# Optimization experiments

Hardware: AMD Instinct MI355X
Metric: run time of the kernel (lower is better)

## Reference

```python
import jax, jax.numpy as jnp
import numpy as np

B, N, D, IN_NF, OUT_NF, H, L = 64, 64, 3, 8, 1, 128, 4
BN = B * N
E = B * N * N


def setup_inputs() -> dict:
    key = jax.random.key(0)
    ks = jax.random.split(key, 12)
    g = lambda k, shape, s=0.05: jax.random.normal(k, shape, jnp.float32) * s
    z = lambda *shape: jnp.zeros(shape, jnp.float32)
    return {
        "xh": jax.random.normal(ks[0], (B, N, D + IN_NF), jnp.float32),
        "node_mask": jnp.ones((B, N, 1), jnp.float32),
        "edge_mask": jnp.ones((B, N * N, 1), jnp.float32),
        "emb_w": g(ks[1], (IN_NF, H)), "emb_b": z(H),
        "out_w": g(ks[2], (H, OUT_NF)), "out_b": z(OUT_NF),
        "ew1": g(ks[3], (L, 2 * H + 2, H)), "eb1": z(L, H),
        "ew2": g(ks[4], (L, H, H)), "eb2": z(L, H),
        "nw1": g(ks[5], (L, 2 * H, H)), "nb1": z(L, H),
        "nw2": g(ks[6], (L, H, H)), "nb2": z(L, H),
        "cw1": g(ks[7], (L, H, H)), "cb1": z(L, H),
        "cw2": g(ks[8], (L, H, 1), 0.001),  # xavier gain 0.001, no bias
    }


def _edges():
    # fully-connected edges within each graph block (matches get_adj_matrix)
    ii = jnp.repeat(jnp.arange(N, dtype=jnp.int32), N)  # source i
    jj = jnp.tile(jnp.arange(N, dtype=jnp.int32), N)    # target j
    offs = (jnp.arange(B, dtype=jnp.int32) * N)[:, None]
    row = (offs + ii[None, :]).reshape(-1)  # [E]
    col = (offs + jj[None, :]).reshape(-1)  # [E]
    return row, col


def reference(xh, node_mask, edge_mask, emb_w, emb_b, out_w, out_b,
              ew1, eb1, ew2, eb2, nw1, nb1, nw2, nb2, cw1, cb1, cw2):
    silu = jax.nn.silu
    row, col = _edges()
    nm = node_mask.reshape(BN, 1)
    em = edge_mask.reshape(E, 1)

    x = xh[:, :, :D].reshape(BN, D) * nm           # coordinates
    h = xh[:, :, D:].reshape(BN, IN_NF) * nm       # node features
    # static per-graph edge attribute: squared distance at input coords
    edge_attr = jnp.sum((x[row] - x[col]) ** 2, axis=1, keepdims=True)  # [E,1]

    h = h @ emb_w + emb_b  # embedding

    for l in range(L):
        coord_diff = x[row] - x[col]                            # [E,D]
        radial = jnp.sum(coord_diff ** 2, axis=1, keepdims=True)  # [E,1]
        coord_diff = coord_diff / (jnp.sqrt(radial + 1e-8) + 1.0)  # norm_diff

        # edge MLP: cat(h_i, h_j, radial, edge_attr) -> SiLU stack
        e_in = jnp.concatenate([h[row], h[col], radial, edge_attr], axis=1)
        m = silu(silu(e_in @ ew1[l] + eb1[l]) @ ew2[l] + eb2[l])  # [E,H]
        m = m * em

        # coordinate update (tanh=False): coord_diff * coord_mlp(m)
        trans = coord_diff * (silu(m @ cw1[l] + cb1[l]) @ cw2[l])  # [E,D]
        trans = trans * em
        x = x + jax.ops.segment_sum(trans, row, num_segments=BN)

        # node update with residual (recurrent=True)
        agg = jax.ops.segment_sum(m, row, num_segments=BN)       # [BN,H]
        n_in = jnp.concatenate([h, agg], axis=1)
        h = h + (silu(n_in @ nw1[l] + nb1[l]) @ nw2[l] + nb2[l])
        h = h * nm

    h = (h @ out_w + out_b) * nm                    # embedding_out + node mask
    return h.reshape(B, N, OUT_NF).mean(axis=1)     # [B, out_nf]
```

## Files before the change

kernel.cpp:

```cpp
#include <hip/hip_runtime.h>
#include <math.h>


#define NB 64
#define NN 64
#define DD 3
#define INNF 8
#define HH 128
#define LL 4
#define BNODES (NB * NN)

typedef __attribute__((ext_vector_type(8))) short bf16x8;
typedef __attribute__((ext_vector_type(4))) float f32x4;

__device__ __forceinline__ float silu_f(float v) {
    float e = __expf(-v);
    return v * __builtin_amdgcn_rcpf(1.0f + e);
}

__device__ __forceinline__ short f2bf(float v) {
    unsigned u = __builtin_bit_cast(unsigned, v);
    u += 0x7fffu + ((u >> 16) & 1u);
    return (short)(u >> 16);
}

__global__ void prep_kernel(const float* __restrict__ xh, const float* __restrict__ nm,
                            const float* __restrict__ emb_w, const float* __restrict__ emb_b,
                            float* __restrict__ x, float* __restrict__ x0, float* __restrict__ h) {
    const int v = blockIdx.x;
    const int t = threadIdx.x;
    const float m = nm[v];
    __shared__ float f[INNF];
    if (t < INNF) f[t] = xh[v * (DD + INNF) + DD + t] * m;
    if (t < DD) {
        float c = xh[v * (DD + INNF) + t] * m;
        x[v * DD + t] = c;
        x0[v * DD + t] = c;
    }
    __syncthreads();
    float acc = emb_b[t];
#pragma unroll
    for (int k = 0; k < INNF; ++k) acc = fmaf(f[k], emb_w[k * HH + t], acc);
    h[v * HH + t] = acc;
}

__global__ void wprep_kernel(const float* __restrict__ ew1, const float* __restrict__ ew2,
                             const float* __restrict__ cw1, const float* __restrict__ nw1,
                             const float* __restrict__ nw2,
                             short* __restrict__ ew1T, short* __restrict__ ew2T,
                             short* __restrict__ cw1T, short* __restrict__ nw1T,
                             short* __restrict__ nw2T) {
    const int l = blockIdx.x / 5, which = blockIdx.x % 5;
    if (which == 0) {
        const float* src = ew1 + (size_t)l * 258 * HH;
        short* dst = ew1T + (size_t)l * 256 * HH;
        for (int idx = threadIdx.x; idx < 256 * HH; idx += blockDim.x) {
            const int cp = idx >> 7, k = idx & 127;
            dst[cp * HH + k] = f2bf(src[(k + ((cp >> 7) << 7)) * HH + (cp & 127)]);
        }
    } else if (which == 3) {
        const float* src = nw1 + (size_t)l * 2 * HH * HH;
        short* dst = nw1T + (size_t)l * 2 * HH * HH;
        for (int idx = threadIdx.x; idx < 2 * HH * HH; idx += blockDim.x) {
            const int c = idx >> 8, k = idx & 255;
            dst[c * 256 + k] = f2bf(src[k * HH + c]);
        }
    } else {
        const float* src = (which == 1 ? ew2 : which == 2 ? cw1 : nw2) + (size_t)l * HH * HH;
        short* dst = (which == 1 ? ew2T : which == 2 ? cw1T : nw2T) + (size_t)l * HH * HH;
        for (int idx = threadIdx.x; idx < HH * HH; idx += blockDim.x) {
            const int k = idx >> 7, c = idx & 127;
            dst[c * HH + k] = f2bf(src[idx]);
        }
    }
}

__global__ __launch_bounds__(256) void pq_kernel(const float* __restrict__ h,
                                                 const short* __restrict__ ew1Tl,
                                                 const float* __restrict__ eb1l,
                                                 float* __restrict__ P, float* __restrict__ Q) {
    const int g0n = (blockIdx.x >> 1) * 16;
    const int half = blockIdx.x & 1;
    const int t = threadIdx.x;
    const int w = t >> 6, l = t & 63, l15 = l & 15, l4 = l >> 4;
    __shared__ __align__(16) char shN[16 * 256];

    {
        const int row = t >> 4, k0 = (t & 15) * 8;
        const float* hp = h + (size_t)(g0n + row) * HH + k0;
        const float4 a = *(const float4*)hp;
        const float4 b = *(const float4*)(hp + 4);
        const float av[8] = {a.x, a.y, a.z, a.w, b.x, b.y, b.z, b.w};
        bf16x8 s;
#pragma unroll
        for (int u = 0; u < 8; ++u) s[u] = f2bf(av[u]);
        *(bf16x8*)(shN + row * 256 + ((k0 * 2) ^ ((row & 7) << 4))) = s;
    }
    __syncthreads();

    const int c0 = half * 128 + w * 32;
    f32x4 acc[2];
    acc[0] = (f32x4){0.f, 0.f, 0.f, 0.f};
    acc[1] = (f32x4){0.f, 0.f, 0.f, 0.f};
#pragma unroll
    for (int kt = 0; kt < 4; ++kt) {
        const bf16x8 af = *(const bf16x8*)(shN + l15 * 256 + (((kt * 4 + l4) * 16) ^ ((l15 & 7) << 4)));
#pragma unroll
        for (int ct2 = 0; ct2 < 2; ++ct2) {
            const bf16x8 bf = *(const bf16x8*)(ew1Tl + (size_t)(c0 + ct2 * 16 + l15) * HH + kt * 32 + l4 * 8);
            acc[ct2] = __builtin_amdgcn_mfma_f32_16x16x32_bf16(af, bf, acc[ct2], 0, 0, 0);
        }
    }
#pragma unroll
    for (int ct2 = 0; ct2 < 2; ++ct2) {
        const int cp = c0 + ct2 * 16 + l15;
        const int c = cp & 127;
        float* dst = (cp >= HH) ? Q : P;
        const float bias = (cp >= HH) ? 0.0f : eb1l[c];
#pragma unroll
        for (int reg = 0; reg < 4; ++reg) {
            const int n = g0n + l4 * 4 + reg;
            dst[(size_t)n * HH + c] = acc[ct2][reg] + bias;
        }
    }
}

__global__ __launch_bounds__(256, 4) void edge_kernel(
    const float* __restrict__ P, const float* __restrict__ Q,
    const float* __restrict__ x, const float* __restrict__ x0,
    const float* __restrict__ em,
    const float* __restrict__ ew1l,
    const short* __restrict__ ew2T,
    const float* __restrict__ eb2l,
    const short* __restrict__ cw1T,
    const float* __restrict__ cb1l,
    const float* __restrict__ cw2l,
    float* __restrict__ x_out, float* __restrict__ agg) {

    const int g  = blockIdx.x >> 5;
    const int ii = blockIdx.x & 31;
    const int iA = ii, iB = ii + 32;
    const int g0 = g * NN;
    const int rA = g0 + iA, rB = g0 + iB;
    const int t = threadIdx.x;
    const int w = t >> 6;
    const int l = t & 63;
    const int l15 = l & 15, l4 = l >> 4;
    const int c0 = w * 32;

    __shared__ __align__(16) char shAc[128 * 256];
    float* shphiP = (float*)(shAc);
    float* shx0g  = (float*)(shAc + 2048);
    __shared__ float shPA[HH], shPB[HH], shw256[HH], shw257[HH];
    __shared__ float shEb2[HH], shCb1[HH], shCw2[HH];
    __shared__ float shx[NN * 3];
    __shared__ float shradA[NN], shradB[NN], sheaA[NN], sheaB[NN], shemA[NN], shemB[NN];
    __shared__ float shcdnA[NN * 3], shcdnB[NN * 3];

    if (t < HH) {
        shPA[t] = P[rA * HH + t];
        shPB[t] = P[rB * HH + t];
        shw256[t] = ew1l[256 * HH + t];
        shw257[t] = ew1l[257 * HH + t];
        shEb2[t] = eb2l[t];
        shCb1[t] = cb1l[t];
        shCw2[t] = cw2l[t];
    }
    if (t < NN * 3) {
        shx[t] = x[g0 * 3 + t];
        shx0g[t] = x0[g0 * 3 + t];
    }
    __syncthreads();
    if (t < 2 * NN) {
        const int j = t & 63;
        const bool isB = (t >= NN);
        const int ni = isB ? iB : iA;
        float dx = shx[ni * 3 + 0] - shx[j * 3 + 0];
        float dy = shx[ni * 3 + 1] - shx[j * 3 + 1];
        float dz = shx[ni * 3 + 2] - shx[j * 3 + 2];
        float rad = dx * dx + dy * dy + dz * dz;
        float inv = 1.0f / (sqrtf(rad + 1e-8f) + 1.0f);
        float ex = shx0g[ni * 3 + 0] - shx0g[j * 3 + 0];
        float ey = shx0g[ni * 3 + 1] - shx0g[j * 3 + 1];
        float ez = shx0g[ni * 3 + 2] - shx0g[j * 3 + 2];
        float ea = ex * ex + ey * ey + ez * ez;
        float* radp = isB ? shradB : shradA;
        float* eap  = isB ? sheaB : sheaA;
        float* emp  = isB ? shemB : shemA;
        float* cdnp = isB ? shcdnB : shcdnA;
        radp[j] = rad;
        eap[j] = ea;
        emp[j] = em[(isB ? rB : rA) * NN + j];
        cdnp[j * 3 + 0] = dx * inv;
        cdnp[j * 3 + 1] = dy * inv;
        cdnp[j * 3 + 2] = dz * inv;
    }
    __syncthreads();

    {
        const int j = t >> 2;
        const float radA = shradA[j], eaA = sheaA[j];
        const float radB = shradB[j], eaB = sheaB[j];
        const int xr = (j & 7) << 4;
#pragma unroll
        for (int p = 0; p < 4; ++p) {
            const int k0 = (t & 3) * 8 + p * 32;
            const float4 qa = *(const float4*)(Q + (size_t)(g0 + j) * HH + k0);
            const float4 qb = *(const float4*)(Q + (size_t)(g0 + j) * HH + k0 + 4);
            const float qv[8] = {qa.x, qa.y, qa.z, qa.w, qb.x, qb.y, qb.z, qb.w};
            bf16x8 sA, sB;
#pragma unroll
            for (int u = 0; u < 8; ++u) {
                const int k = k0 + u;
                const float w2 = shw256[k], w3 = shw257[k];
                float vA = shPA[k] + qv[u] + radA * w2 + eaA * w3;
                float vB = shPB[k] + qv[u] + radB * w2 + eaB * w3;
                sA[u] = f2bf(silu_f(vA));
                sB[u] = f2bf(silu_f(vB));
            }
            const int off = (k0 * 2) ^ xr;
            *(bf16x8*)(shAc + j * 256 + off) = sA;
            *(bf16x8*)(shAc + (j + 64) * 256 + off) = sB;
        }
    }
    __syncthreads();

    f32x4 acc[8][2];
#pragma unroll
    for (int rt = 0; rt < 8; ++rt) {
        acc[rt][0] = (f32x4){0.f, 0.f, 0.f, 0.f};
        acc[rt][1] = (f32x4){0.f, 0.f, 0.f, 0.f};
    }
    {
        const short* B2 = ew2T + (size_t)(c0 + l15) * HH + l4 * 8;
        bf16x8 bcur[2], bnxt[2];
        bcur[0] = *(const bf16x8*)(B2);
        bcur[1] = *(const bf16x8*)(B2 + 16 * HH);
#pragma unroll
        for (int kt = 0; kt < 4; ++kt) {
            if (kt < 3) {
                bnxt[0] = *(const bf16x8*)(B2 + (kt + 1) * 32);
                bnxt[1] = *(const bf16x8*)(B2 + 16 * HH + (kt + 1) * 32);
            }
            bf16x8 af[8];
#pragma unroll
            for (int rt = 0; rt < 8; ++rt) {
                const int row = rt * 16 + l15;
                af[rt] = *(const bf16x8*)(shAc + row * 256 + (((kt * 4 + l4) * 16) ^ ((row & 7) << 4)));
            }
#pragma unroll
            for (int rt = 0; rt < 8; ++rt) {
                acc[rt][0] = __builtin_amdgcn_mfma_f32_16x16x32_bf16(af[rt], bcur[0], acc[rt][0], 0, 0, 0);
                acc[rt][1] = __builtin_amdgcn_mfma_f32_16x16x32_bf16(af[rt], bcur[1], acc[rt][1], 0, 0, 0);
            }
            bcur[0] = bnxt[0];
            bcur[1] = bnxt[1];
        }
    }
    __syncthreads();

#pragma unroll
    for (int ct2 = 0; ct2 < 2; ++ct2) {
        const int c = c0 + ct2 * 16 + l15;
        const float b = shEb2[c];
        float paggA = 0.0f, paggB = 0.0f;
#pragma unroll
        for (int rt = 0; rt < 8; ++rt) {
#pragma unroll
            for (int reg = 0; reg < 4; ++reg) {
                const int row = rt * 16 + l4 * 4 + reg;
                const float emv = (rt < 4) ? shemA[row] : shemB[row - 64];
                float v = silu_f(acc[rt][ct2][reg] + b) * emv;
                if (rt < 4) paggA += v; else paggB += v;
                const int byte = row * 256 + ((c * 2) ^ ((row & 7) << 4));
                *(short*)(shAc + byte) = f2bf(v);
            }
        }
        paggA += __shfl_xor(paggA, 16);
        paggA += __shfl_xor(paggA, 32);
        paggB += __shfl_xor(paggB, 16);
        paggB += __shfl_xor(paggB, 32);
        if (l4 == 0) {
            agg[rA * HH + c] = paggA;
            agg[rB * HH + c] = paggB;
        }
    }
    __syncthreads();

#pragma unroll
    for (int rt = 0; rt < 8; ++rt) {
        acc[rt][0] = (f32x4){0.f, 0.f, 0.f, 0.f};
        acc[rt][1] = (f32x4){0.f, 0.f, 0.f, 0.f};
    }
    {
        const short* B3 = cw1T + (size_t)(c0 + l15) * HH + l4 * 8;
        bf16x8 bcur[2], bnxt[2];
        bcur[0] = *(const bf16x8*)(B3);
        bcur[1] = *(const bf16x8*)(B3 + 16 * HH);
#pragma unroll
        for (int kt = 0; kt < 4; ++kt) {
            if (kt < 3) {
                bnxt[0] = *(const bf16x8*)(B3 + (kt + 1) * 32);
                bnxt[1] = *(const bf16x8*)(B3 + 16 * HH + (kt + 1) * 32);
            }
            bf16x8 af[8];
#pragma unroll
            for (int rt = 0; rt < 8; ++rt) {
                const int row = rt * 16 + l15;
                af[rt] = *(const bf16x8*)(shAc + row * 256 + (((kt * 4 + l4) * 16) ^ ((row & 7) << 4)));
            }
#pragma unroll
            for (int rt = 0; rt < 8; ++rt) {
                acc[rt][0] = __builtin_amdgcn_mfma_f32_16x16x32_bf16(af[rt], bcur[0], acc[rt][0], 0, 0, 0);
                acc[rt][1] = __builtin_amdgcn_mfma_f32_16x16x32_bf16(af[rt], bcur[1], acc[rt][1], 0, 0, 0);
            }
            bcur[0] = bnxt[0];
            bcur[1] = bnxt[1];
        }
    }

    float pp[8][4];
    {
#pragma unroll
        for (int rt = 0; rt < 8; ++rt)
#pragma unroll
            for (int reg = 0; reg < 4; ++reg) pp[rt][reg] = 0.0f;
#pragma unroll
        for (int ct2 = 0; ct2 < 2; ++ct2) {
            const int c = c0 + ct2 * 16 + l15;
            const float cb = shCb1[c], cw = shCw2[c];
#pragma unroll
            for (int rt = 0; rt < 8; ++rt) {
#pragma unroll
                for (int reg = 0; reg < 4; ++reg) {
                    float v = silu_f(acc[rt][ct2][reg] + cb);
                    pp[rt][reg] = fmaf(v, cw, pp[rt][reg]);
                }
            }
        }
#pragma unroll
        for (int off = 8; off >= 1; off >>= 1) {
#pragma unroll
            for (int rt = 0; rt < 8; ++rt)
#pragma unroll
                for (int reg = 0; reg < 4; ++reg) pp[rt][reg] += __shfl_xor(pp[rt][reg], off);
        }
    }
    __syncthreads();
    if (l15 == 0) {
#pragma unroll
        for (int rt = 0; rt < 8; ++rt)
#pragma unroll
            for (int reg = 0; reg < 4; ++reg)
                shphiP[w * 128 + rt * 16 + l4 * 4 + reg] = pp[rt][reg];
    }
    __syncthreads();

    if (t < 192) {
        const int q = t >> 6, j = t & 63;
        float phiA = shphiP[0 * 128 + j] + shphiP[1 * 128 + j] + shphiP[2 * 128 + j] + shphiP[3 * 128 + j];
        float vA = shcdnA[j * 3 + q] * phiA * shemA[j];
        float phiB = shphiP[0 * 128 + 64 + j] + shphiP[1 * 128 + 64 + j] + shphiP[2 * 128 + 64 + j] + shphiP[3 * 128 + 64 + j];
        float vB = shcdnB[j * 3 + q] * phiB * shemB[j];
#pragma unroll
        for (int off = 32; off >= 1; off >>= 1) {
            vA += __shfl_xor(vA, off);
            vB += __shfl_xor(vB, off);
        }
        if (j == 0) {
            x_out[rA * 3 + q] = shx[iA * 3 + q] + vA;
            x_out[rB * 3 + q] = shx[iB * 3 + q] + vB;
        }
    }
}

__global__ __launch_bounds__(256) void node_kernel(float* __restrict__ h, const float* __restrict__ agg,
                            const float* __restrict__ nm,
                            const short* __restrict__ nw1Tl, const float* __restrict__ nb1l,
                            const short* __restrict__ nw2Tl, const float* __restrict__ nb2l) {
    const int g0n = blockIdx.x * 16;
    const int t = threadIdx.x;
    const int w = t >> 6, l = t & 63, l15 = l & 15, l4 = l >> 4;
    __shared__ __align__(16) char shN[16 * 512];
    __shared__ __align__(16) char shT[16 * 256];

    {
        const int row = t >> 4, k0 = (t & 15) * 16;
        const float* src = (k0 < HH) ? (h + (size_t)(g0n + row) * HH + k0)
                                     : (agg + (size_t)(g0n + row) * HH + (k0 - HH));
        const float4 a = *(const float4*)src;
        const float4 b = *(const float4*)(src + 4);
        const float4 c = *(const float4*)(src + 8);
        const float4 d = *(const float4*)(src + 12);
        const float av[16] = {a.x, a.y, a.z, a.w, b.x, b.y, b.z, b.w,
                              c.x, c.y, c.z, c.w, d.x, d.y, d.z, d.w};
        bf16x8 s0, s1;
#pragma unroll
        for (int u = 0; u < 8; ++u) { s0[u] = f2bf(av[u]); s1[u] = f2bf(av[8 + u]); }
        const int xr = (row & 7) << 4;
        *(bf16x8*)(shN + row * 512 + ((k0 * 2) ^ xr)) = s0;
        *(bf16x8*)(shN + row * 512 + ((k0 * 2 + 16) ^ xr)) = s1;
    }
    __syncthreads();

    const int c0 = w * 32;
    f32x4 acc[2];
    acc[0] = (f32x4){0.f, 0.f, 0.f, 0.f};
    acc[1] = (f32x4){0.f, 0.f, 0.f, 0.f};
#pragma unroll
    for (int kt = 0; kt < 8; ++kt) {
        const bf16x8 af = *(const bf16x8*)(shN + l15 * 512 + (((kt * 4 + l4) * 16) ^ ((l15 & 7) << 4)));
#pragma unroll
        for (int ct2 = 0; ct2 < 2; ++ct2) {
            const bf16x8 bf = *(const bf16x8*)(nw1Tl + (size_t)(c0 + ct2 * 16 + l15) * 256 + kt * 32 + l4 * 8);
            acc[ct2] = __builtin_amdgcn_mfma_f32_16x16x32_bf16(af, bf, acc[ct2], 0, 0, 0);
        }
    }
#pragma unroll
    for (int ct2 = 0; ct2 < 2; ++ct2) {
        const int c = c0 + ct2 * 16 + l15;
        const float b = nb1l[c];
#pragma unroll
        for (int reg = 0; reg < 4; ++reg) {
            const int row = l4 * 4 + reg;
            const float v = silu_f(acc[ct2][reg] + b);
            *(short*)(shT + row * 256 + ((c * 2) ^ ((row & 7) << 4))) = f2bf(v);
        }
    }
    __syncthreads();

    acc[0] = (f32x4){0.f, 0.f, 0.f, 0.f};
    acc[1] = (f32x4){0.f, 0.f, 0.f, 0.f};
#pragma unroll
    for (int kt = 0; kt < 4; ++kt) {
        const bf16x8 af = *(const bf16x8*)(shT + l15 * 256 + (((kt * 4 + l4) * 16) ^ ((l15 & 7) << 4)));
#pragma unroll
        for (int ct2 = 0; ct2 < 2; ++ct2) {
            const bf16x8 bf = *(const bf16x8*)(nw2Tl + (size_t)(c0 + ct2 * 16 + l15) * HH + kt * 32 + l4 * 8);
            acc[ct2] = __builtin_amdgcn_mfma_f32_16x16x32_bf16(af, bf, acc[ct2], 0, 0, 0);
        }
    }
#pragma unroll
    for (int ct2 = 0; ct2 < 2; ++ct2) {
        const int c = c0 + ct2 * 16 + l15;
        const float b = nb2l[c];
#pragma unroll
        for (int reg = 0; reg < 4; ++reg) {
            const int n = g0n + l4 * 4 + reg;
            const float hv = h[(size_t)n * HH + c];
            h[(size_t)n * HH + c] = (hv + acc[ct2][reg] + b) * nm[n];
        }
    }
}

__global__ void out_kernel(const float* __restrict__ h, const float* __restrict__ nm,
                           const float* __restrict__ ow, const float* __restrict__ ob,
                           float* __restrict__ out) {
    const int b = blockIdx.x;
    const int n = threadIdx.x;
    const int v = b * NN + n;
    float acc = 0.0f;
#pragma unroll 8
    for (int c = 0; c < HH; ++c) acc = fmaf(h[v * HH + c], ow[c], acc);
    acc = (acc + ob[0]) * nm[v];
#pragma unroll
    for (int off = 32; off >= 1; off >>= 1) acc += __shfl_xor(acc, off);
    if (n == 0) out[b] = acc * (1.0f / (float)NN);
}

extern "C" void kernel_launch(void* const* d_in, const int* in_sizes, int n_in,
                              void* d_out, int out_size, void* d_ws, size_t ws_size,
                              hipStream_t stream) {
    const float* xh    = (const float*)d_in[0];
    const float* nmask = (const float*)d_in[1];
    const float* emask = (const float*)d_in[2];
    const float* emb_w = (const float*)d_in[3];
    const float* emb_b = (const float*)d_in[4];
    const float* out_w = (const float*)d_in[5];
    const float* out_b = (const float*)d_in[6];
    const float* ew1   = (const float*)d_in[7];
    const float* eb1   = (const float*)d_in[8];
    const float* ew2   = (const float*)d_in[9];
    const float* eb2   = (const float*)d_in[10];
    const float* nw1   = (const float*)d_in[11];
    const float* nb1   = (const float*)d_in[12];
    const float* nw2   = (const float*)d_in[13];
    const float* nb2   = (const float*)d_in[14];
    const float* cw1   = (const float*)d_in[15];
    const float* cb1   = (const float*)d_in[16];
    const float* cw2   = (const float*)d_in[17];

    float* ws  = (float*)d_ws;
    float* xA  = ws;
    float* xB  = xA + BNODES * 3;
    float* x0  = xB + BNODES * 3;
    float* h   = x0 + BNODES * 3;
    float* Pb  = h + BNODES * HH;
    float* Qb  = Pb + BNODES * HH;
    float* agg = Qb + BNODES * HH;
    short* ew2T = (short*)(agg + BNODES * HH);
    short* cw1T = ew2T + LL * HH * HH;
    short* ew1T = cw1T + LL * HH * HH;
    short* nw1T = ew1T + LL * 256 * HH;
    short* nw2T = nw1T + LL * 256 * HH;

    prep_kernel<<<BNODES, HH, 0, stream>>>(xh, nmask, emb_w, emb_b, xA, x0, h);
    wprep_kernel<<<5 * LL, 256, 0, stream>>>(ew1, ew2, cw1, nw1, nw2,
                                             ew1T, ew2T, cw1T, nw1T, nw2T);

    float* xc = xA;
    float* xn = xB;
    for (int l = 0; l < LL; ++l) {
        const float* ew1l = ew1 + (size_t)l * 258 * HH;
        pq_kernel<<<512, 256, 0, stream>>>(h, ew1T + (size_t)l * 256 * HH, eb1 + l * HH, Pb, Qb);
        edge_kernel<<<BNODES / 2, 256, 0, stream>>>(Pb, Qb, xc, x0, emask, ew1l,
                                                    ew2T + (size_t)l * HH * HH, eb2 + l * HH,
                                                    cw1T + (size_t)l * HH * HH, cb1 + l * HH,
                                                    cw2 + (size_t)l * HH, xn, agg);
        node_kernel<<<256, 256, 0, stream>>>(h, agg, nmask,
                                             nw1T + (size_t)l * 2 * HH * HH, nb1 + l * HH,
                                             nw2T + (size_t)l * HH * HH, nb2 + l * HH);
        float* tmp = xc; xc = xn; xn = tmp;
    }

    out_kernel<<<NB, NN, 0, stream>>>(h, nmask, out_w, out_b, (float*)d_out);
}
```

Before: 296.5 us.

## Fuse next-layer P/Q projection into node kernel and use packed bf16 conversion

Folds the per-layer P/Q edge-input projection into the tail of the node update kernel, so the freshly updated h is converted to bf16 in shared memory and multiplied by the next layer's ew1 without a separate launch or a reload of h. Only the first layer keeps a standalone pq launch. Separately, scalar software float-to-bf16 rounding is replaced with the hardware v_cvt_pk_bf16_f32 instruction, which packs two values at once. The fusion removes three launches and one pass over h, but adds a barrier and extra MFMA work to a 256-block node kernel. That kernel has lower parallelism than the 512-block pq launch it replaces.

```diff
diff --git a/kernel.cpp b/kernel.cpp
--- a/kernel.cpp
+++ b/kernel.cpp
@@ -12,6 +12,7 @@
 
 typedef __attribute__((ext_vector_type(8))) short bf16x8;
 typedef __attribute__((ext_vector_type(4))) float f32x4;
+typedef __attribute__((ext_vector_type(4))) unsigned uint32x4;
 
 __device__ __forceinline__ float silu_f(float v) {
     float e = __expf(-v);
@@ -22,6 +23,12 @@
     unsigned u = __builtin_bit_cast(unsigned, v);
     u += 0x7fffu + ((u >> 16) & 1u);
     return (short)(u >> 16);
+}
+
+__device__ __forceinline__ unsigned cvt_pk2(float lo, float hi) {
+    unsigned r;
+    asm("v_cvt_pk_bf16_f32 %0, %1, %2" : "=v"(r) : "v"(lo), "v"(hi));
+    return r;
 }
 
 __global__ void prep_kernel(const float* __restrict__ xh, const float* __restrict__ nm,
@@ -90,11 +97,12 @@
         const float* hp = h + (size_t)(g0n + row) * HH + k0;
         const float4 a = *(const float4*)hp;
         const float4 b = *(const float4*)(hp + 4);
-        const float av[8] = {a.x, a.y, a.z, a.w, b.x, b.y, b.z, b.w};
-        bf16x8 s;
-#pragma unroll
-        for (int u = 0; u < 8; ++u) s[u] = f2bf(av[u]);
-        *(bf16x8*)(shN + row * 256 + ((k0 * 2) ^ ((row & 7) << 4))) = s;
+        uint32x4 s;
+        s[0] = cvt_pk2(a.x, a.y);
+        s[1] = cvt_pk2(a.z, a.w);
+        s[2] = cvt_pk2(b.x, b.y);
+        s[3] = cvt_pk2(b.z, b.w);
+        *(uint32x4*)(shN + row * 256 + ((k0 * 2) ^ ((row & 7) << 4))) = s;
     }
     __syncthreads();
 
@@ -208,19 +216,22 @@
             const float4 qa = *(const float4*)(Q + (size_t)(g0 + j) * HH + k0);
             const float4 qb = *(const float4*)(Q + (size_t)(g0 + j) * HH + k0 + 4);
             const float qv[8] = {qa.x, qa.y, qa.z, qa.w, qb.x, qb.y, qb.z, qb.w};
-            bf16x8 sA, sB;
-#pragma unroll
-            for (int u = 0; u < 8; ++u) {
-                const int k = k0 + u;
-                const float w2 = shw256[k], w3 = shw257[k];
-                float vA = shPA[k] + qv[u] + radA * w2 + eaA * w3;
-                float vB = shPB[k] + qv[u] + radB * w2 + eaB * w3;
-                sA[u] = f2bf(silu_f(vA));
-                sB[u] = f2bf(silu_f(vB));
+            uint32x4 sA, sB;
+#pragma unroll
+            for (int u2 = 0; u2 < 4; ++u2) {
+                const int ka = k0 + 2 * u2, kb = ka + 1;
+                const float w2a = shw256[ka], w3a = shw257[ka];
+                const float w2b = shw256[kb], w3b = shw257[kb];
+                float vA0 = silu_f(shPA[ka] + qv[2 * u2] + radA * w2a + eaA * w3a);
+                float vA1 = silu_f(shPA[kb] + qv[2 * u2 + 1] + radA * w2b + eaA * w3b);
+                float vB0 = silu_f(shPB[ka] + qv[2 * u2] + radB * w2a + eaB * w3a);
+                float vB1 = silu_f(shPB[kb] + qv[2 * u2 + 1] + radB * w2b + eaB * w3b);
+                sA[u2] = cvt_pk2(vA0, vA1);
+                sB[u2] = cvt_pk2(vB0, vB1);
             }
             const int off = (k0 * 2) ^ xr;
-            *(bf16x8*)(shAc + j * 256 + off) = sA;
-            *(bf16x8*)(shAc + (j + 64) * 256 + off) = sB;
+            *(uint32x4*)(shAc + j * 256 + off) = sA;
+            *(uint32x4*)(shAc + (j + 64) * 256 + off) = sB;
         }
     }
     __syncthreads();
@@ -266,14 +277,24 @@
         float paggA = 0.0f, paggB = 0.0f;
 #pragma unroll
         for (int rt = 0; rt < 8; ++rt) {
+            const int rbase = rt * 16 + l4 * 4;
+            float v[4];
 #pragma unroll
             for (int reg = 0; reg < 4; ++reg) {
-                const int row = rt * 16 + l4 * 4 + reg;
+                const int row = rbase + reg;
                 const float emv = (rt < 4) ? shemA[row] : shemB[row - 64];
-                float v = silu_f(acc[rt][ct2][reg] + b) * emv;
-                if (rt < 4) paggA += v; else paggB += v;
-                const int byte = row * 256 + ((c * 2) ^ ((row & 7) << 4));
-                *(short*)(shAc + byte) = f2bf(v);
+                v[reg] = silu_f(acc[rt][ct2][reg] + b) * emv;
+                if (rt < 4) paggA += v[reg]; else paggB += v[reg];
+            }
+            const unsigned wlo = cvt_pk2(v[0], v[1]);
+            const unsigned whi = cvt_pk2(v[2], v[3]);
+            const int cx = c * 2;
+#pragma unroll
+            for (int reg = 0; reg < 4; ++reg) {
+                const int row = rbase + reg;
+                const unsigned wv = (reg < 2) ? wlo : whi;
+                const short sv = (reg & 1) ? (short)(wv >> 16) : (short)(wv & 0xffff);
+                *(short*)(shAc + row * 256 + (cx ^ ((row & 7) << 4))) = sv;
             }
         }
         paggA += __shfl_xor(paggA, 16);
@@ -374,15 +395,18 @@
     }
 }
 
-__global__ __launch_bounds__(256) void node_kernel(float* __restrict__ h, const float* __restrict__ agg,
-                            const float* __restrict__ nm,
-                            const short* __restrict__ nw1Tl, const float* __restrict__ nb1l,
-                            const short* __restrict__ nw2Tl, const float* __restrict__ nb2l) {
+__global__ __launch_bounds__(256) void nodepq_kernel(
+    float* __restrict__ h, const float* __restrict__ agg, const float* __restrict__ nm,
+    const short* __restrict__ nw1Tl, const float* __restrict__ nb1l,
+    const short* __restrict__ nw2Tl, const float* __restrict__ nb2l,
+    const short* __restrict__ ew1Tn, const float* __restrict__ eb1n,
+    float* __restrict__ P, float* __restrict__ Q, int do_pq) {
     const int g0n = blockIdx.x * 16;
     const int t = threadIdx.x;
     const int w = t >> 6, l = t & 63, l15 = l & 15, l4 = l >> 4;
     __shared__ __align__(16) char shN[16 * 512];
     __shared__ __align__(16) char shT[16 * 256];
+    char* shH = shN;
 
     {
         const int row = t >> 4, k0 = (t & 15) * 16;
@@ -392,14 +416,14 @@
         const float4 b = *(const float4*)(src + 4);
         const float4 c = *(const float4*)(src + 8);
         const float4 d = *(const float4*)(src + 12);
-        const float av[16] = {a.x, a.y, a.z, a.w, b.x, b.y, b.z, b.w,
-                              c.x, c.y, c.z, c.w, d.x, d.y, d.z, d.w};
-        bf16x8 s0, s1;
-#pragma unroll
-        for (int u = 0; u < 8; ++u) { s0[u] = f2bf(av[u]); s1[u] = f2bf(av[8 + u]); }
+        uint32x4 s0, s1;
+        s0[0] = cvt_pk2(a.x, a.y); s0[1] = cvt_pk2(a.z, a.w);
+        s0[2] = cvt_pk2(b.x, b.y); s0[3] = cvt_pk2(b.z, b.w);
+        s1[0] = cvt_pk2(c.x, c.y); s1[1] = cvt_pk2(c.z, c.w);
+        s1[2] = cvt_pk2(d.x, d.y); s1[3] = cvt_pk2(d.z, d.w);
         const int xr = (row & 7) << 4;
-        *(bf16x8*)(shN + row * 512 + ((k0 * 2) ^ xr)) = s0;
-        *(bf16x8*)(shN + row * 512 + ((k0 * 2 + 16) ^ xr)) = s1;
+        *(uint32x4*)(shN + row * 512 + ((k0 * 2) ^ xr)) = s0;
+        *(uint32x4*)(shN + row * 512 + ((k0 * 2 + 16) ^ xr)) = s1;
     }
     __syncthreads();
 
@@ -416,15 +440,22 @@
             acc[ct2] = __builtin_amdgcn_mfma_f32_16x16x32_bf16(af, bf, acc[ct2], 0, 0, 0);
         }
     }
+    __syncthreads();
 #pragma unroll
     for (int ct2 = 0; ct2 < 2; ++ct2) {
         const int c = c0 + ct2 * 16 + l15;
         const float b = nb1l[c];
+        float v[4];
+#pragma unroll
+        for (int reg = 0; reg < 4; ++reg) v[reg] = silu_f(acc[ct2][reg] + b);
+        const unsigned wlo = cvt_pk2(v[0], v[1]);
+        const unsigned whi = cvt_pk2(v[2], v[3]);
 #pragma unroll
         for (int reg = 0; reg < 4; ++reg) {
             const int row = l4 * 4 + reg;
-            const float v = silu_f(acc[ct2][reg] + b);
-            *(short*)(shT + row * 256 + ((c * 2) ^ ((row & 7) << 4))) = f2bf(v);
+            const unsigned wv = (reg < 2) ? wlo : whi;
+            const short sv = (reg & 1) ? (short)(wv >> 16) : (short)(wv & 0xffff);
+            *(short*)(shT + row * 256 + ((c * 2) ^ ((row & 7) << 4))) = sv;
         }
     }
     __syncthreads();
@@ -440,6 +471,7 @@
             acc[ct2] = __builtin_amdgcn_mfma_f32_16x16x32_bf16(af, bf, acc[ct2], 0, 0, 0);
         }
     }
+    float hn[2][4];
 #pragma unroll
     for (int ct2 = 0; ct2 < 2; ++ct2) {
         const int c = c0 + ct2 * 16 + l15;
@@ -448,7 +480,58 @@
         for (int reg = 0; reg < 4; ++reg) {
             const int n = g0n + l4 * 4 + reg;
             const float hv = h[(size_t)n * HH + c];
-            h[(size_t)n * HH + c] = (hv + acc[ct2][reg] + b) * nm[n];
+            hn[ct2][reg] = (hv + acc[ct2][reg] + b) * nm[n];
+            h[(size_t)n * HH + c] = hn[ct2][reg];
+        }
+    }
+    if (!do_pq) return;
+
+#pragma unroll
+    for (int ct2 = 0; ct2 < 2; ++ct2) {
+        const int c = c0 + ct2 * 16 + l15;
+        const unsigned wlo = cvt_pk2(hn[ct2][0], hn[ct2][1]);
+        const unsigned whi = cvt_pk2(hn[ct2][2], hn[ct2][3]);
+#pragma unroll
+        for (int reg = 0; reg < 4; ++reg) {
+            const int row = l4 * 4 + reg;
+            const unsigned wv = (reg < 2) ? wlo : whi;
+            const short sv = (reg & 1) ? (short)(wv >> 16) : (short)(wv & 0xffff);
+            *(short*)(shH + row * 256 + ((c * 2) ^ ((row & 7) << 4))) = sv;
+        }
+    }
+    __syncthreads();
+
+    f32x4 pacc[2][2];
+#pragma unroll
+    for (int half = 0; half < 2; ++half) {
+        pacc[half][0] = (f32x4){0.f, 0.f, 0.f, 0.f};
+        pacc[half][1] = (f32x4){0.f, 0.f, 0.f, 0.f};
+    }
+#pragma unroll
+    for (int kt = 0; kt < 4; ++kt) {
+        const bf16x8 af = *(const bf16x8*)(shH + l15 * 256 + (((kt * 4 + l4) * 16) ^ ((l15 & 7) << 4)));
+#pragma unroll
+        for (int half = 0; half < 2; ++half) {
+#pragma unroll
+            for (int ct2 = 0; ct2 < 2; ++ct2) {
+                const bf16x8 bf = *(const bf16x8*)(ew1Tn + (size_t)(half * 128 + c0 + ct2 * 16 + l15) * HH + kt * 32 + l4 * 8);
+                pacc[half][ct2] = __builtin_amdgcn_mfma_f32_16x16x32_bf16(af, bf, pacc[half][ct2], 0, 0, 0);
+            }
+        }
+    }
+#pragma unroll
+    for (int half = 0; half < 2; ++half) {
+#pragma unroll
+        for (int ct2 = 0; ct2 < 2; ++ct2) {
+            const int cp = half * 128 + c0 + ct2 * 16 + l15;
+            const int c = cp & 127;
+            float* dst = (cp >= HH) ? Q : P;
+            const float bias = (cp >= HH) ? 0.0f : eb1n[c];
+#pragma unroll
+            for (int reg = 0; reg < 4; ++reg) {
+                const int n = g0n + l4 * 4 + reg;
+                dst[(size_t)n * HH + c] = pacc[half][ct2][reg] + bias;
+            }
         }
     }
 }
@@ -508,18 +591,23 @@
     wprep_kernel<<<5 * LL, 256, 0, stream>>>(ew1, ew2, cw1, nw1, nw2,
                                              ew1T, ew2T, cw1T, nw1T, nw2T);
 
+    pq_kernel<<<512, 256, 0, stream>>>(h, ew1T, eb1, Pb, Qb);
+
     float* xc = xA;
     float* xn = xB;
     for (int l = 0; l < LL; ++l) {
         const float* ew1l = ew1 + (size_t)l * 258 * HH;
-        pq_kernel<<<512, 256, 0, stream>>>(h, ew1T + (size_t)l * 256 * HH, eb1 + l * HH, Pb, Qb);
         edge_kernel<<<BNODES / 2, 256, 0, stream>>>(Pb, Qb, xc, x0, emask, ew1l,
                                                     ew2T + (size_t)l * HH * HH, eb2 + l * HH,
                                                     cw1T + (size_t)l * HH * HH, cb1 + l * HH,
                                                     cw2 + (size_t)l * HH, xn, agg);
-        node_kernel<<<256, 256, 0, stream>>>(h, agg, nmask,
-                                             nw1T + (size_t)l * 2 * HH * HH, nb1 + l * HH,
-                                             nw2T + (size_t)l * HH * HH, nb2 + l * HH);
+        const int do_pq = (l + 1 < LL) ? 1 : 0;
+        const int ln = do_pq ? (l + 1) : 0;
+        nodepq_kernel<<<256, 256, 0, stream>>>(h, agg, nmask,
+                                               nw1T + (size_t)l * 2 * HH * HH, nb1 + l * HH,
+                                               nw2T + (size_t)l * HH * HH, nb2 + l * HH,
+                                               ew1T + (size_t)ln * 256 * HH, eb1 + ln * HH,
+                                               Pb, Qb, do_pq);
         float* tmp = xc; xc = xn; xn = tmp;
     }
 
```

Result: faster. 284.5 us (-4.0%).
